# Optimization experiments

Hardware: AMD Instinct MI355X
Metric: run time of the kernel (lower is better)

## Reference

```python
import jax, jax.numpy as jnp
import numpy as np

B, LD, LP, DIM = 8, 128, 1000, 128
LN_EPS = 1e-5


def layer_norm(x, gamma, beta, eps=LN_EPS):
    mu = jnp.mean(x, axis=-1, keepdims=True)
    var = jnp.mean(jnp.square(x - mu), axis=-1, keepdims=True)
    return (x - mu) * jax.lax.rsqrt(var + eps) * gamma + beta


def setup_inputs() -> dict:
    key = jax.random.key(0)
    ks = jax.random.split(key, 8)
    s = 1.0 / np.sqrt(DIM)
    return {
        "drug_conv": jax.random.normal(ks[0], (B, LD, DIM), dtype=jnp.float32),
        "protein_conv": jax.random.normal(ks[1], (B, LP, DIM), dtype=jnp.float32),
        "W_d": jax.random.normal(ks[2], (DIM, DIM), dtype=jnp.float32) * s,
        "b_d": jnp.zeros((DIM,), dtype=jnp.float32),
        "W_p": jax.random.normal(ks[3], (DIM, DIM), dtype=jnp.float32) * s,
        "b_p": jnp.zeros((DIM,), dtype=jnp.float32),
        "W_att": jax.random.normal(ks[4], (DIM, DIM), dtype=jnp.float32) * s,
        "b_att": jnp.zeros((DIM,), dtype=jnp.float32),
        "gamma1": jnp.ones((DIM,), dtype=jnp.float32),
        "beta1": jnp.zeros((DIM,), dtype=jnp.float32),
        "gamma2": jnp.ones((DIM,), dtype=jnp.float32),
        "beta2": jnp.zeros((DIM,), dtype=jnp.float32),
    }


def reference(drug_conv, protein_conv, W_d, b_d, W_p, b_p, W_att, b_att,
              gamma1, beta1, gamma2, beta2):
    # drug_conv: (B, LD, DIM), protein_conv: (B, LP, DIM)
    d_att = drug_conv @ W_d.T + b_d        # (B, LD, DIM)
    p_att = protein_conv @ W_p.T + b_p     # (B, LP, DIM)
    # Pairwise additive interaction (B, LD, LP, DIM) -- the fusable hotspot.
    M = jax.nn.relu(d_att[:, :, None, :] + p_att[:, None, :, :])
    # Linear commutes with mean: apply attention_layer after reduction.
    compound_att = jax.nn.sigmoid(jnp.mean(M, axis=2) @ W_att.T + b_att)  # (B, LD, DIM)
    protein_att = jax.nn.sigmoid(jnp.mean(M, axis=1) @ W_att.T + b_att)   # (B, LP, DIM)
    drug = drug_conv * 0.5 + drug_conv * compound_att
    prot = protein_conv * 0.5 + protein_conv * protein_att
    # MaxPool1d over full length axis == max over L, then LayerNorm(dim).
    drug_vec = layer_norm(jnp.max(drug, axis=1), gamma1, beta1)   # (B, DIM)
    prot_vec = layer_norm(jnp.max(prot, axis=1), gamma2, beta2)   # (B, DIM)
    return (drug_vec, prot_vec)
```

## Files before the change

### kernel.cpp

```cpp
#include <hip/hip_runtime.h>
#include <math.h>

#define B 8
#define LD 128
#define LP 1000
#define DIM 128
#define R 8
#define LN_EPS 1e-5f

#define NBLK_D (B * LD / R)
#define NBLK_P (B * LP / R)
#define SEG_D (NBLK_D / B)
#define SEG_P (NBLK_P / B)

__global__ void gemv_both(const float* __restrict__ Xd, const float* __restrict__ Xp,
                          const float* __restrict__ Wd, const float* __restrict__ bd,
                          const float* __restrict__ Wp, const float* __restrict__ bp,
                          float* __restrict__ outd, float* __restrict__ outp) {
    const int blk = blockIdx.x;
    const int t = threadIdx.x;

    const float *X, *W, *bias;
    float* out;
    int row0;
    if (blk < NBLK_D) { X = Xd; W = Wd; bias = bd; out = outd; row0 = blk * R; }
    else              { X = Xp; W = Wp; bias = bp; out = outp; row0 = (blk - NBLK_D) * R; }

    __shared__ float4 xs4[R][DIM / 4];
    float* xs = (float*)xs4;
#pragma unroll
    for (int r = 0; r < R; ++r) xs[r * DIM + t] = X[(row0 + r) * DIM + t];
    __syncthreads();

    float acc[R];
    const float bv = bias[t];
#pragma unroll
    for (int r = 0; r < R; ++r) acc[r] = bv;

    const float4* w4 = reinterpret_cast<const float4*>(W + t * DIM);
#pragma unroll
    for (int k = 0; k < DIM / 4; ++k) {
        const float4 w = w4[k];
#pragma unroll
        for (int r = 0; r < R; ++r) {
            const float4 x = xs4[r][k];
            acc[r] += w.x * x.x + w.y * x.y + w.z * x.z + w.w * x.w;
        }
    }
#pragma unroll
    for (int r = 0; r < R; ++r) out[(row0 + r) * DIM + t] = acc[r];
}

__global__ void pairwise(const float* __restrict__ d_att, const float* __restrict__ p_att,
                         float* __restrict__ Mc, float* __restrict__ Mp) {
    const int blk = blockIdx.x;
    const int b = blk >> 7;
    const int d = blk & (DIM - 1);
    const int t = threadIdx.x;

    __shared__ float xs[LD];
    __shared__ float ys[LP];
    __shared__ float red[256];

    for (int i = t; i < LD; i += 256) xs[i] = d_att[(b * LD + i) * DIM + d];
    for (int j = t; j < LP; j += 256) ys[j] = p_att[(b * LP + j) * DIM + d];
    __syncthreads();

    for (int j = t; j < LP; j += 256) {
        const float y = ys[j];
        float s = 0.f;
#pragma unroll 8
        for (int i = 0; i < LD; ++i) s += fmaxf(0.f, xs[i] + y);
        Mp[(b * LP + j) * DIM + d] = s * (1.f / (float)LD);
    }

    {
        const int r = t & (LD - 1);
        const int h = t >> 7;
        const float x = xs[r];
        float s = 0.f;
        const int j0 = h * (LP / 2);
#pragma unroll 4
        for (int jj = 0; jj < LP / 2; ++jj) s += fmaxf(0.f, x + ys[j0 + jj]);
        red[t] = s;
    }
    __syncthreads();
    if (t < LD) {
        Mc[(b * LD + t) * DIM + d] = (red[t] + red[t + LD]) * (1.f / (float)LP);
    }
}

__global__ void gated_both(const float* __restrict__ Mc, const float* __restrict__ Mp,
                           const float* __restrict__ W, const float* __restrict__ bias,
                           const float* __restrict__ convd, const float* __restrict__ convp,
                           float* __restrict__ pd, float* __restrict__ pp) {
    const int blk = blockIdx.x;
    const int t = threadIdx.x;

    const float *M, *conv;
    float* part;
    int row0;
    if (blk < NBLK_D) { M = Mc; conv = convd; part = pd + blk * DIM; row0 = blk * R; }
    else { const int pb = blk - NBLK_D; M = Mp; conv = convp; part = pp + pb * DIM; row0 = pb * R; }

    __shared__ float4 xs4[R][DIM / 4];
    float* xs = (float*)xs4;
#pragma unroll
    for (int r = 0; r < R; ++r) xs[r * DIM + t] = M[(row0 + r) * DIM + t];
    __syncthreads();

    float acc[R];
    const float bv = bias[t];
#pragma unroll
    for (int r = 0; r < R; ++r) acc[r] = bv;

    const float4* w4 = reinterpret_cast<const float4*>(W + t * DIM);
#pragma unroll
    for (int k = 0; k < DIM / 4; ++k) {
        const float4 w = w4[k];
#pragma unroll
        for (int r = 0; r < R; ++r) {
            const float4 x = xs4[r][k];
            acc[r] += w.x * x.x + w.y * x.y + w.z * x.z + w.w * x.w;
        }
    }

    float m = -INFINITY;
#pragma unroll
    for (int r = 0; r < R; ++r) {
        const float att = 1.f / (1.f + expf(-acc[r]));
        const float v = conv[(row0 + r) * DIM + t] * (0.5f + att);
        m = fmaxf(m, v);
    }
    part[t] = m;
}

__global__ void maxln_final(const float* __restrict__ pd, const float* __restrict__ pp,
                            const float* __restrict__ gamma1, const float* __restrict__ beta1,
                            const float* __restrict__ gamma2, const float* __restrict__ beta2,
                            float* __restrict__ out) {
    const int blk = blockIdx.x;
    const int kind = blk >> 3;
    const int b = blk & 7;
    const int t = threadIdx.x;

    float m = -INFINITY;
    if (kind == 0) {
        const float* base = pd + b * SEG_D * DIM;
#pragma unroll
        for (int s = 0; s < SEG_D; ++s) m = fmaxf(m, base[s * DIM + t]);
    } else {
        const float* base = pp + b * SEG_P * DIM;
#pragma unroll 5
        for (int s = 0; s < SEG_P; ++s) m = fmaxf(m, base[s * DIM + t]);
    }

    __shared__ float s1[DIM];
    __shared__ float s2[DIM];
    s1[t] = m;
    s2[t] = m * m;
    __syncthreads();
    for (int off = DIM / 2; off > 0; off >>= 1) {
        if (t < off) { s1[t] += s1[t + off]; s2[t] += s2[t + off]; }
        __syncthreads();
    }
    const float mu = s1[0] * (1.f / (float)DIM);
    const float var = s2[0] * (1.f / (float)DIM) - mu * mu;
    const float inv = rsqrtf(var + LN_EPS);

    const float* gamma = kind ? gamma2 : gamma1;
    const float* beta  = kind ? beta2  : beta1;
    out[blk * DIM + t] = (m - mu) * inv * gamma[t] + beta[t];
}

extern "C" void kernel_launch(void* const* d_in, const int* in_sizes, int n_in,
                              void* d_out, int out_size, void* d_ws, size_t ws_size,
                              hipStream_t stream) {
    const float* drug_conv    = (const float*)d_in[0];
    const float* protein_conv = (const float*)d_in[1];
    const float* W_d   = (const float*)d_in[2];
    const float* b_d   = (const float*)d_in[3];
    const float* W_p   = (const float*)d_in[4];
    const float* b_p   = (const float*)d_in[5];
    const float* W_att = (const float*)d_in[6];
    const float* b_att = (const float*)d_in[7];
    const float* gamma1 = (const float*)d_in[8];
    const float* beta1  = (const float*)d_in[9];
    const float* gamma2 = (const float*)d_in[10];
    const float* beta2  = (const float*)d_in[11];
    float* out = (float*)d_out;

    float* ws = (float*)d_ws;
    const size_t n_datt = (size_t)B * LD * DIM;
    const size_t n_patt = (size_t)B * LP * DIM;
    float* d_att = ws;
    float* p_att = ws + n_datt;
    float* Mc    = ws + n_datt + n_patt;
    float* Mp    = ws + n_datt + n_patt + n_datt;
    float* pd = ws;
    float* pp = ws + (size_t)NBLK_D * DIM;

    gemv_both<<<NBLK_D + NBLK_P, DIM, 0, stream>>>(drug_conv, protein_conv,
                                                   W_d, b_d, W_p, b_p, d_att, p_att);
    pairwise<<<B * DIM, 256, 0, stream>>>(d_att, p_att, Mc, Mp);
    gated_both<<<NBLK_D + NBLK_P, DIM, 0, stream>>>(Mc, Mp, W_att, b_att,
                                                    drug_conv, protein_conv, pd, pp);
    maxln_final<<<16, DIM, 0, stream>>>(pd, pp, gamma1, beta1, gamma2, beta2, out);
}
```

Before: 153.9 us.

## Register-block pairwise reductions, vectorize row loads, split final max across threads

The pairwise kernel now has each thread handle two protein positions with a float2 read of a padded shared array. The drug-side reduction is restructured so each thread accumulates four drug rows over strided protein chunks, followed by an 8-way shared reduction. This is meant to cut shared-memory reads per ReLU-add and balance work across threads. The gemv/gated kernels also switch to float4 row loads, launch bounds are added, and the final max-reduce uses 256 threads, at the cost of padding logic and an extra sync.

```diff
diff --git a/kernel.cpp b/kernel.cpp
--- a/kernel.cpp
+++ b/kernel.cpp
@@ -4,6 +4,7 @@
 #define B 8
 #define LD 128
 #define LP 1000
+#define LP_PAD 1008
 #define DIM 128
 #define R 8
 #define LN_EPS 1e-5f
@@ -13,10 +14,11 @@
 #define SEG_D (NBLK_D / B)
 #define SEG_P (NBLK_P / B)
 
-__global__ void gemv_both(const float* __restrict__ Xd, const float* __restrict__ Xp,
-                          const float* __restrict__ Wd, const float* __restrict__ bd,
-                          const float* __restrict__ Wp, const float* __restrict__ bp,
-                          float* __restrict__ outd, float* __restrict__ outp) {
+__global__ __launch_bounds__(DIM) void gemv_both(
+        const float* __restrict__ Xd, const float* __restrict__ Xp,
+        const float* __restrict__ Wd, const float* __restrict__ bd,
+        const float* __restrict__ Wp, const float* __restrict__ bp,
+        float* __restrict__ outd, float* __restrict__ outp) {
     const int blk = blockIdx.x;
     const int t = threadIdx.x;
 
@@ -27,9 +29,12 @@
     else              { X = Xp; W = Wp; bias = bp; out = outp; row0 = (blk - NBLK_D) * R; }
 
     __shared__ float4 xs4[R][DIM / 4];
-    float* xs = (float*)xs4;
-#pragma unroll
-    for (int r = 0; r < R; ++r) xs[r * DIM + t] = X[(row0 + r) * DIM + t];
+    {
+        const float4* Xv = reinterpret_cast<const float4*>(X + (size_t)row0 * DIM);
+        float4* s = (float4*)xs4;
+        s[t] = Xv[t];
+        s[t + DIM] = Xv[t + DIM];
+    }
     __syncthreads();
 
     float acc[R];
@@ -51,49 +56,72 @@
     for (int r = 0; r < R; ++r) out[(row0 + r) * DIM + t] = acc[r];
 }
 
-__global__ void pairwise(const float* __restrict__ d_att, const float* __restrict__ p_att,
-                         float* __restrict__ Mc, float* __restrict__ Mp) {
+__global__ __launch_bounds__(256) void pairwise(
+        const float* __restrict__ d_att, const float* __restrict__ p_att,
+        float* __restrict__ Mc, float* __restrict__ Mp) {
     const int blk = blockIdx.x;
     const int b = blk >> 7;
     const int d = blk & (DIM - 1);
     const int t = threadIdx.x;
 
     __shared__ float xs[LD];
-    __shared__ float ys[LP];
-    __shared__ float red[256];
-
-    for (int i = t; i < LD; i += 256) xs[i] = d_att[(b * LD + i) * DIM + d];
-    for (int j = t; j < LP; j += 256) ys[j] = p_att[(b * LP + j) * DIM + d];
-    __syncthreads();
-
-    for (int j = t; j < LP; j += 256) {
-        const float y = ys[j];
+    __shared__ float2 ys2[LP_PAD / 2];
+    __shared__ float red[LD * 8];
+
+    if (t < LD) xs[t] = d_att[(b * LD + t) * DIM + d];
+    for (int j = t; j < LP_PAD; j += 256) {
+        ((float*)ys2)[j] = (j < LP) ? p_att[(b * LP + j) * DIM + d] : -1e30f;
+    }
+    __syncthreads();
+
+    for (int p = t; p < LP_PAD / 2; p += 256) {
+        const float2 y = ys2[p];
+        float2 acc = make_float2(0.f, 0.f);
+#pragma unroll 8
+        for (int i = 0; i < LD; ++i) {
+            const float x = xs[i];
+            acc.x += fmaxf(0.f, x + y.x);
+            acc.y += fmaxf(0.f, x + y.y);
+        }
+        const int j = 2 * p;
+        if (j < LP)     Mp[(b * LP + j) * DIM + d]     = acc.x * (1.f / (float)LD);
+        if (j + 1 < LP) Mp[(b * LP + j + 1) * DIM + d] = acc.y * (1.f / (float)LD);
+    }
+
+    {
+        const int rq = t >> 3;
+        const int sl = t & 7;
+        const float x0 = xs[4 * rq + 0];
+        const float x1 = xs[4 * rq + 1];
+        const float x2 = xs[4 * rq + 2];
+        const float x3 = xs[4 * rq + 3];
+        float2 a0 = make_float2(0.f, 0.f), a1 = a0, a2 = a0, a3 = a0;
+        for (int p = sl; p < LP_PAD / 2; p += 8) {
+            const float2 y = ys2[p];
+            a0.x += fmaxf(0.f, x0 + y.x); a0.y += fmaxf(0.f, x0 + y.y);
+            a1.x += fmaxf(0.f, x1 + y.x); a1.y += fmaxf(0.f, x1 + y.y);
+            a2.x += fmaxf(0.f, x2 + y.x); a2.y += fmaxf(0.f, x2 + y.y);
+            a3.x += fmaxf(0.f, x3 + y.x); a3.y += fmaxf(0.f, x3 + y.y);
+        }
+        red[(4 * rq + 0) * 8 + sl] = a0.x + a0.y;
+        red[(4 * rq + 1) * 8 + sl] = a1.x + a1.y;
+        red[(4 * rq + 2) * 8 + sl] = a2.x + a2.y;
+        red[(4 * rq + 3) * 8 + sl] = a3.x + a3.y;
+    }
+    __syncthreads();
+    if (t < LD) {
         float s = 0.f;
-#pragma unroll 8
-        for (int i = 0; i < LD; ++i) s += fmaxf(0.f, xs[i] + y);
-        Mp[(b * LP + j) * DIM + d] = s * (1.f / (float)LD);
-    }
-
-    {
-        const int r = t & (LD - 1);
-        const int h = t >> 7;
-        const float x = xs[r];
-        float s = 0.f;
-        const int j0 = h * (LP / 2);
-#pragma unroll 4
-        for (int jj = 0; jj < LP / 2; ++jj) s += fmaxf(0.f, x + ys[j0 + jj]);
-        red[t] = s;
-    }
-    __syncthreads();
-    if (t < LD) {
-        Mc[(b * LD + t) * DIM + d] = (red[t] + red[t + LD]) * (1.f / (float)LP);
-    }
-}
-
-__global__ void gated_both(const float* __restrict__ Mc, const float* __restrict__ Mp,
-                           const float* __restrict__ W, const float* __restrict__ bias,
-                           const float* __restrict__ convd, const float* __restrict__ convp,
-                           float* __restrict__ pd, float* __restrict__ pp) {
+#pragma unroll
+        for (int k = 0; k < 8; ++k) s += red[t * 8 + k];
+        Mc[(b * LD + t) * DIM + d] = s * (1.f / (float)LP);
+    }
+}
+
+__global__ __launch_bounds__(DIM) void gated_both(
+        const float* __restrict__ Mc, const float* __restrict__ Mp,
+        const float* __restrict__ W, const float* __restrict__ bias,
+        const float* __restrict__ convd, const float* __restrict__ convp,
+        float* __restrict__ pd, float* __restrict__ pp) {
     const int blk = blockIdx.x;
     const int t = threadIdx.x;
 
@@ -104,9 +132,12 @@
     else { const int pb = blk - NBLK_D; M = Mp; conv = convp; part = pp + pb * DIM; row0 = pb * R; }
 
     __shared__ float4 xs4[R][DIM / 4];
-    float* xs = (float*)xs4;
-#pragma unroll
-    for (int r = 0; r < R; ++r) xs[r * DIM + t] = M[(row0 + r) * DIM + t];
+    {
+        const float4* Mv = reinterpret_cast<const float4*>(M + (size_t)row0 * DIM);
+        float4* s = (float4*)xs4;
+        s[t] = Mv[t];
+        s[t + DIM] = Mv[t + DIM];
+    }
     __syncthreads();
 
     float acc[R];
@@ -135,42 +166,55 @@
     part[t] = m;
 }
 
-__global__ void maxln_final(const float* __restrict__ pd, const float* __restrict__ pp,
-                            const float* __restrict__ gamma1, const float* __restrict__ beta1,
-                            const float* __restrict__ gamma2, const float* __restrict__ beta2,
-                            float* __restrict__ out) {
+__global__ __launch_bounds__(256) void maxln_final(
+        const float* __restrict__ pd, const float* __restrict__ pp,
+        const float* __restrict__ gamma1, const float* __restrict__ beta1,
+        const float* __restrict__ gamma2, const float* __restrict__ beta2,
+        float* __restrict__ out) {
     const int blk = blockIdx.x;
     const int kind = blk >> 3;
     const int b = blk & 7;
-    const int t = threadIdx.x;
+    const int t = threadIdx.x & (DIM - 1);
+    const int h = threadIdx.x >> 7;
 
     float m = -INFINITY;
     if (kind == 0) {
         const float* base = pd + b * SEG_D * DIM;
-#pragma unroll
-        for (int s = 0; s < SEG_D; ++s) m = fmaxf(m, base[s * DIM + t]);
+        for (int s = h; s < SEG_D; s += 2) m = fmaxf(m, base[s * DIM + t]);
     } else {
         const float* base = pp + b * SEG_P * DIM;
-#pragma unroll 5
-        for (int s = 0; s < SEG_P; ++s) m = fmaxf(m, base[s * DIM + t]);
-    }
+        for (int s = h; s < SEG_P; s += 2) m = fmaxf(m, base[s * DIM + t]);
+    }
+
+    __shared__ float sm[2][DIM];
+    sm[h][t] = m;
+    __syncthreads();
 
     __shared__ float s1[DIM];
     __shared__ float s2[DIM];
-    s1[t] = m;
-    s2[t] = m * m;
+    if (threadIdx.x < DIM) {
+        m = fmaxf(sm[0][t], sm[1][t]);
+        sm[0][t] = m;
+        s1[t] = m;
+        s2[t] = m * m;
+    }
     __syncthreads();
     for (int off = DIM / 2; off > 0; off >>= 1) {
-        if (t < off) { s1[t] += s1[t + off]; s2[t] += s2[t + off]; }
+        if (threadIdx.x < off) {
+            s1[threadIdx.x] += s1[threadIdx.x + off];
+            s2[threadIdx.x] += s2[threadIdx.x + off];
+        }
         __syncthreads();
     }
-    const float mu = s1[0] * (1.f / (float)DIM);
-    const float var = s2[0] * (1.f / (float)DIM) - mu * mu;
-    const float inv = rsqrtf(var + LN_EPS);
-
-    const float* gamma = kind ? gamma2 : gamma1;
-    const float* beta  = kind ? beta2  : beta1;
-    out[blk * DIM + t] = (m - mu) * inv * gamma[t] + beta[t];
+    if (threadIdx.x < DIM) {
+        const float mu = s1[0] * (1.f / (float)DIM);
+        const float var = s2[0] * (1.f / (float)DIM) - mu * mu;
+        const float inv = rsqrtf(var + LN_EPS);
+        const float* gamma = kind ? gamma2 : gamma1;
+        const float* beta  = kind ? beta2  : beta1;
+        const float mv = sm[0][t];
+        out[blk * DIM + t] = (mv - mu) * inv * gamma[t] + beta[t];
+    }
 }
 
 extern "C" void kernel_launch(void* const* d_in, const int* in_sizes, int n_in,
@@ -205,5 +249,5 @@
     pairwise<<<B * DIM, 256, 0, stream>>>(d_att, p_att, Mc, Mp);
     gated_both<<<NBLK_D + NBLK_P, DIM, 0, stream>>>(Mc, Mp, W_att, b_att,
                                                     drug_conv, protein_conv, pd, pp);
-    maxln_final<<<16, DIM, 0, stream>>>(pd, pp, gamma1, beta1, gamma2, beta2, out);
-}
+    maxln_final<<<16, 256, 0, stream>>>(pd, pp, gamma1, beta1, gamma2, beta2, out);
+}
```

Result: faster. 145.6 us (-5.4%).
